# Performance work log

Measured on AMD Instinct MI355X. Metric: run time of the kernel, lower is better.

The kernel has to match this reference:

```python
import jax, jax.numpy as jnp
import numpy as np

B, S, H, F, E, K = 2, 2048, 1024, 4096, 8, 2


def setup_inputs() -> dict:
    key = jax.random.key(0)
    ks = jax.random.split(key, 5)
    scale = 0.02
    return {
        "hidden_states": jax.random.normal(ks[0], (B, S, H), jnp.float32),
        "gate_w": jax.random.normal(ks[1], (H, E), jnp.float32) * scale,  # nn.Linear(H,E,bias=False)
        "w1": jax.random.normal(ks[2], (E, H, F), jnp.float32) * scale,   # per-expert fc1
        "b1": jnp.zeros((E, F), jnp.float32),
        "w2": jax.random.normal(ks[3], (E, F, H), jnp.float32) * scale,   # per-expert fc2
        "b2": jnp.zeros((E, H), jnp.float32),
    }


def reference(hidden_states, gate_w, w1, b1, w2, b2):
    b, s, h = hidden_states.shape
    x = hidden_states.reshape(b * s, h)  # [T, H]
    T = x.shape[0]
    n_experts = gate_w.shape[1]

    # --- Top-K gating ---
    router_logits = x @ gate_w                      # [T, E]
    router_probs = jax.nn.softmax(router_logits, axis=-1)
    topk_probs, topk_idx = jax.lax.top_k(router_probs, K)  # [T, K]
    topk_probs = topk_probs / topk_probs.sum(axis=-1, keepdims=True)
    aux_loss = n_experts * jnp.sum(router_probs.mean(axis=0) ** 2)

    # --- Combine weights: scatter normalized top-k probs into dense [T, E] ---
    combine_w = jnp.zeros((T, n_experts), x.dtype).at[
        jnp.arange(T)[:, None], topk_idx
    ].add(topk_probs)

    # --- Expert MLPs (dense per-expert batched GEMM; zero combine weight drops unrouted) ---
    hidden = jax.nn.relu(jnp.einsum('th,ehf->etf', x, w1) + b1[:, None, :])  # [E, T, F]
    expert_out = jnp.einsum('etf,efh->eth', hidden, w2) + b2[:, None, :]     # [E, T, H]

    out = jnp.einsum('te,eth->th', combine_w, expert_out)  # weighted combine
    return out.reshape(b, s, h), aux_loss
```

## Files before the change

### kernel.cpp

```cpp
#include <hip/hip_runtime.h>
#include <hip/hip_bf16.h>
#include <cstdint>

#define AS1 __attribute__((address_space(1)))
#define AS3 __attribute__((address_space(3)))

typedef __attribute__((ext_vector_type(8))) short short8x;
typedef __attribute__((ext_vector_type(4))) float f32x4;

static constexpr int T    = 4096;
static constexpr int HD   = 1024;
static constexpr int FD   = 4096;
static constexpr int NE   = 8;
static constexpr int P    = T * 2;
static constexpr int PPAD = P + 128;
static constexpr int MAXT = P / 128 + NE;
static constexpr int RTB  = 16;
static constexpr int RNB  = T / RTB;

struct TileDesc { int e; int start; int rows; int pad; };

__device__ __forceinline__ uint16_t f2bf(float f) {
  uint32_t u = __builtin_bit_cast(uint32_t, f);
  u += 0x7FFFu + ((u >> 16) & 1u);
  return (uint16_t)(u >> 16);
}
__device__ __forceinline__ float bf2f(uint16_t b) {
  uint32_t u = ((uint32_t)b) << 16;
  return __builtin_bit_cast(float, u);
}
__device__ __forceinline__ void gload_lds16(const void* g, void* l) {
  __builtin_amdgcn_global_load_lds((const AS1 uint32_t*)g, (AS3 uint32_t*)l, 16, 0, 0);
}

__global__ __launch_bounds__(256) void cvt_x_kernel(const float* __restrict__ x,
                                                    uint16_t* __restrict__ xb) {
  size_t i = ((size_t)blockIdx.x * 256 + threadIdx.x) * 4;
  float4 v = *(const float4*)&x[i];
  ushort4 o;
  o.x = f2bf(v.x); o.y = f2bf(v.y); o.z = f2bf(v.z); o.w = f2bf(v.w);
  *(ushort4*)&xb[i] = o;
}

__global__ __launch_bounds__(256) void transpose_cvt_kernel(
    const float* __restrict__ in, uint16_t* __restrict__ out, int R, int C) {
  __shared__ float tile[64][65];
  int z = blockIdx.z;
  const float* inp = in + (size_t)z * R * C;
  uint16_t* outp = out + (size_t)z * R * C;
  int r0 = blockIdx.y * 64, c0 = blockIdx.x * 64;
  int tid = threadIdx.x;
  int lr = tid >> 4;
  int lc4 = (tid & 15) * 4;
#pragma unroll
  for (int p = 0; p < 4; ++p) {
    float4 v = *(const float4*)&inp[(size_t)(r0 + lr + p * 16) * C + c0 + lc4];
    tile[lr + p * 16][lc4 + 0] = v.x;
    tile[lr + p * 16][lc4 + 1] = v.y;
    tile[lr + p * 16][lc4 + 2] = v.z;
    tile[lr + p * 16][lc4 + 3] = v.w;
  }
  __syncthreads();
#pragma unroll
  for (int p = 0; p < 4; ++p) {
    int c = lr + p * 16;
    ushort4 o;
    o.x = f2bf(tile[lc4 + 0][c]);
    o.y = f2bf(tile[lc4 + 1][c]);
    o.z = f2bf(tile[lc4 + 2][c]);
    o.w = f2bf(tile[lc4 + 3][c]);
    *(ushort4*)&outp[(size_t)(c0 + c) * R + r0 + lc4] = o;
  }
}

__global__ __launch_bounds__(256) void router_kernel(
    const float* __restrict__ x, const float* __restrict__ gate_w,
    int* __restrict__ topk_idx, float* __restrict__ topk_w,
    float* __restrict__ part_sums, int* __restrict__ part_counts) {
  __shared__ float g[NE * HD];
  __shared__ float ls[NE];
  __shared__ int   lc[NE];
  int tid = threadIdx.x;
  for (int i = tid; i < NE * HD; i += 256)
    g[(i & 7) * HD + (i >> 3)] = gate_w[i];
  if (tid < NE) { ls[tid] = 0.f; lc[tid] = 0; }
  __syncthreads();
  int wave = tid >> 6, lane = tid & 63;
  float psum[NE];
#pragma unroll
  for (int e = 0; e < NE; ++e) psum[e] = 0.f;

  for (int tt = 0; tt < RTB / 4; ++tt) {
    int t = blockIdx.x * RTB + wave * (RTB / 4) + tt;
    const float* xr = x + (size_t)t * HD;
    float acc[NE];
#pragma unroll
    for (int e = 0; e < NE; ++e) acc[e] = 0.f;
    for (int i = 0; i < HD / 64; ++i) {
      float xv = xr[lane + i * 64];
#pragma unroll
      for (int e = 0; e < NE; ++e) acc[e] += xv * g[e * HD + lane + i * 64];
    }
#pragma unroll
    for (int off = 32; off > 0; off >>= 1)
#pragma unroll
      for (int e = 0; e < NE; ++e) acc[e] += __shfl_down(acc[e], off);
    if (lane == 0) {
      float m = acc[0];
#pragma unroll
      for (int e = 1; e < NE; ++e) m = fmaxf(m, acc[e]);
      float p[NE], s = 0.f;
#pragma unroll
      for (int e = 0; e < NE; ++e) { p[e] = expf(acc[e] - m); s += p[e]; }
      float inv = 1.f / s;
#pragma unroll
      for (int e = 0; e < NE; ++e) { p[e] *= inv; psum[e] += p[e]; }
      int i0 = 0;
#pragma unroll
      for (int e = 1; e < NE; ++e) if (p[e] > p[i0]) i0 = e;
      int i1 = (i0 == 0) ? 1 : 0;
#pragma unroll
      for (int e = 0; e < NE; ++e) if (e != i0 && e != i1 && p[e] > p[i1]) i1 = e;
      float wsum = p[i0] + p[i1];
      topk_idx[t * 2] = i0; topk_idx[t * 2 + 1] = i1;
      topk_w[t * 2] = p[i0] / wsum; topk_w[t * 2 + 1] = p[i1] / wsum;
      atomicAdd(&lc[i0], 1); atomicAdd(&lc[i1], 1);
    }
  }
  if (lane == 0)
#pragma unroll
    for (int e = 0; e < NE; ++e) atomicAdd(&ls[e], psum[e]);
  __syncthreads();
  if (tid < NE) {
    part_sums[blockIdx.x * NE + tid]   = ls[tid];
    part_counts[blockIdx.x * NE + tid] = lc[tid];
  }
}

__global__ __launch_bounds__(64) void finalize_kernel(
    const int* __restrict__ part_counts, const float* __restrict__ part_sums,
    int* __restrict__ offsets, TileDesc* __restrict__ desc,
    int* __restrict__ ntiles, float* __restrict__ aux_out) {
  __shared__ int   csh[NE];
  __shared__ float ssh[NE];
  int tid = threadIdx.x;
  if (tid < NE) {
    int c = 0; float s = 0.f;
    for (int b = 0; b < RNB; ++b) {
      c += part_counts[b * NE + tid];
      s += part_sums[b * NE + tid];
    }
    csh[tid] = c; ssh[tid] = s;
  }
  __syncthreads();
  if (tid == 0) {
    int off = 0, nt = 0;
    for (int e = 0; e < NE; ++e) {
      offsets[e] = off;
      int c = csh[e];
      for (int i = 0; i < c; i += 128) {
        int rows = c - i; if (rows > 128) rows = 128;
        desc[nt].e = e; desc[nt].start = off + i; desc[nt].rows = rows; desc[nt].pad = 0;
        nt++;
      }
      off += c;
    }
    *ntiles = nt;
    float aux = 0.f;
    for (int e = 0; e < NE; ++e) {
      float mean = ssh[e] / (float)T;
      aux += mean * mean;
    }
    *aux_out = (float)NE * aux;
  }
}

__global__ __launch_bounds__(256) void scatter_kernel(
    const int* __restrict__ topk_idx, const int* __restrict__ offsets,
    int* __restrict__ fill, int* __restrict__ pair_tok, int* __restrict__ tok_pos) {
  int t = blockIdx.x * 256 + threadIdx.x;
  int lane = threadIdx.x & 63;
  unsigned long long below = (lane == 63) ? ~0ull >> 1
                                          : ((1ull << (lane + 1)) - 1) >> 1;
#pragma unroll
  for (int k = 0; k < 2; ++k) {
    int e = topk_idx[t * 2 + k];
    int pos = 0;
    for (int ex = 0; ex < NE; ++ex) {
      unsigned long long m = __ballot(e == ex);
      if (e == ex) {
        int leader = __ffsll((long long)m) - 1;
        int cnt = __popcll(m);
        int base = 0;
        if (lane == leader) base = atomicAdd(&fill[ex], cnt);
        base = __shfl(base, leader);
        pos = base + __popcll(m & below);
      }
    }
    int pp = offsets[e] + pos;
    pair_tok[pp] = t;
    tok_pos[t * 2 + k] = pp;
  }
}

template <int KD, int ND, int NBG, int EPI>
__global__ __launch_bounds__(256) void moe_gemm(
    const uint16_t* __restrict__ Abase, const int* __restrict__ pair_tok,
    const uint16_t* __restrict__ Bw, const float* __restrict__ bias,
    uint16_t* __restrict__ Cout, const TileDesc* __restrict__ desc,
    const int* __restrict__ ntiles) {
  constexpr int NB = ND / 128;
  constexpr int SM = MAXT / 8;

  int orig = blockIdx.x;
  int xcd = orig & 7, local = orig >> 3;
  int nbq = local / (SM * NBG);
  int rem = local % (SM * NBG);
  int mt  = xcd * SM + rem / NBG;
  int nb  = nbq * NBG + rem % NBG;
  if (mt >= *ntiles) return;
  TileDesc d = desc[mt];

  __shared__ uint16_t As[128 * 32];
  __shared__ uint16_t Bs[128 * 32];
  __shared__ int rowA[128];

  int tid = threadIdx.x, lane = tid & 63, wave = tid >> 6;
  int wm = wave >> 1, wn = wave & 1;

  int idx0 = (wave * 2 + 0) * 64 + lane;
  int idx1 = (wave * 2 + 1) * 64 + lane;
  int ar0 = idx0 >> 2, kc0 = idx0 & 3;
  int ar1 = idx1 >> 2, kc1 = idx1 & 3;

  int ra0, ra1;
  if constexpr (EPI == 0) {
    if (tid < 128) rowA[tid] = (tid < d.rows) ? pair_tok[d.start + tid] : 0;
    __syncthreads();
    ra0 = rowA[ar0]; ra1 = rowA[ar1];
  } else {
    ra0 = d.start + ar0; ra1 = d.start + ar1;
  }

  const uint16_t* Bbase = Bw + ((size_t)d.e * ND + (size_t)nb * 128) * KD;

  f32x4 acc[4][4];
#pragma unroll
  for (int i = 0; i < 4; ++i)
#pragma unroll
    for (int j = 0; j < 4; ++j) acc[i][j] = (f32x4){0.f, 0.f, 0.f, 0.f};

  for (int kt = 0; kt < KD / 32; ++kt) {
    if (kt) __syncthreads();
    int kb = kt * 32;
    gload_lds16(Abase + (size_t)ra0 * KD + kb + kc0 * 8, &As[(wave * 2 + 0) * 512]);
    gload_lds16(Abase + (size_t)ra1 * KD + kb + kc1 * 8, &As[(wave * 2 + 1) * 512]);
    gload_lds16(Bbase + (size_t)ar0 * KD + kb + kc0 * 8, &Bs[(wave * 2 + 0) * 512]);
    gload_lds16(Bbase + (size_t)ar1 * KD + kb + kc1 * 8, &Bs[(wave * 2 + 1) * 512]);
    __syncthreads();

    short8x af[4], bfr[4];
#pragma unroll
    for (int i = 0; i < 4; ++i)
      af[i] = *(const short8x*)&As[(wm * 64 + i * 16 + (lane & 15)) * 32 + (lane >> 4) * 8];
#pragma unroll
    for (int j = 0; j < 4; ++j)
      bfr[j] = *(const short8x*)&Bs[(wn * 64 + j * 16 + (lane & 15)) * 32 + (lane >> 4) * 8];
#pragma unroll
    for (int i = 0; i < 4; ++i)
#pragma unroll
      for (int j = 0; j < 4; ++j)
        acc[i][j] = __builtin_amdgcn_mfma_f32_16x16x32_bf16(af[i], bfr[j], acc[i][j], 0, 0, 0);
  }

  int rq = (lane >> 4) * 4;
  int cl = lane & 15;
#pragma unroll
  for (int i = 0; i < 4; ++i) {
    int rb = wm * 64 + i * 16 + rq;
#pragma unroll
    for (int j = 0; j < 4; ++j) {
      int col = nb * 128 + wn * 64 + j * 16 + cl;
      float bv = bias[d.e * ND + col];
#pragma unroll
      for (int q = 0; q < 4; ++q) {
        int r = rb + q;
        if (r < d.rows) {
          float v = acc[i][j][q] + bv;
          if (EPI == 0) v = fmaxf(v, 0.f);
          Cout[(size_t)(d.start + r) * ND + col] = f2bf(v);
        }
      }
    }
  }
}

__global__ __launch_bounds__(256) void combine_kernel(
    const uint16_t* __restrict__ po, const int* __restrict__ tok_pos,
    const float* __restrict__ topk_w, float* __restrict__ out) {
  int t = blockIdx.x;
  int c = threadIdx.x * 4;
  int p0 = tok_pos[t * 2], p1 = tok_pos[t * 2 + 1];
  float w0 = topk_w[t * 2], w1 = topk_w[t * 2 + 1];
  ushort4 a = *(const ushort4*)&po[(size_t)p0 * HD + c];
  ushort4 b = *(const ushort4*)&po[(size_t)p1 * HD + c];
  float4 o;
  o.x = w0 * bf2f(a.x) + w1 * bf2f(b.x);
  o.y = w0 * bf2f(a.y) + w1 * bf2f(b.y);
  o.z = w0 * bf2f(a.z) + w1 * bf2f(b.z);
  o.w = w0 * bf2f(a.w) + w1 * bf2f(b.w);
  *(float4*)&out[(size_t)t * HD + c] = o;
}

extern "C" void kernel_launch(void* const* d_in, const int* in_sizes, int n_in,
                              void* d_out, int out_size, void* d_ws, size_t ws_size,
                              hipStream_t stream) {
  const float* x      = (const float*)d_in[0];
  const float* gate_w = (const float*)d_in[1];
  const float* w1     = (const float*)d_in[2];
  const float* b1     = (const float*)d_in[3];
  const float* w2     = (const float*)d_in[4];
  const float* b2     = (const float*)d_in[5];
  float* out = (float*)d_out;
  (void)in_sizes; (void)n_in; (void)out_size; (void)ws_size;

  char* w = (char*)d_ws;
  size_t off = 0;
  auto alloc = [&](size_t bytes) -> void* {
    void* p = w + off;
    off = (off + bytes + 255) & ~(size_t)255;
    return p;
  };
  int*      meta     = (int*)alloc(256);
  int*      fill     = meta;
  int*      offsets  = (int*)alloc(256);
  int*      ntiles   = offsets + 8;
  TileDesc* desc     = (TileDesc*)alloc(sizeof(TileDesc) * 128);
  int*      topk_idx = (int*)alloc(sizeof(int) * P);
  float*    topk_w   = (float*)alloc(sizeof(float) * P);
  int*      tok_pos  = (int*)alloc(sizeof(int) * P);
  int*      pair_tok = (int*)alloc(sizeof(int) * PPAD);
  float*    psums    = (float*)alloc(sizeof(float) * RNB * NE);
  int*      pcounts  = (int*)alloc(sizeof(int) * RNB * NE);
  uint16_t* xb       = (uint16_t*)alloc((size_t)T * HD * 2);
  uint16_t* w1t      = (uint16_t*)alloc((size_t)NE * FD * HD * 2);
  uint16_t* w2t      = (uint16_t*)alloc((size_t)NE * HD * FD * 2);
  uint16_t* hidden   = (uint16_t*)alloc((size_t)PPAD * FD * 2);
  uint16_t* pout     = (uint16_t*)alloc((size_t)PPAD * HD * 2);

  hipMemsetAsync(meta, 0, 256, stream);
  cvt_x_kernel<<<(T * HD) / 1024, 256, 0, stream>>>(x, xb);
  transpose_cvt_kernel<<<dim3(FD / 64, HD / 64, NE), 256, 0, stream>>>(w1, w1t, HD, FD);
  transpose_cvt_kernel<<<dim3(HD / 64, FD / 64, NE), 256, 0, stream>>>(w2, w2t, FD, HD);
  router_kernel<<<RNB, 256, 0, stream>>>(x, gate_w, topk_idx, topk_w, psums, pcounts);
  finalize_kernel<<<1, 64, 0, stream>>>(pcounts, psums, offsets, desc, ntiles,
                                        out + (size_t)T * HD);
  scatter_kernel<<<T / 256, 256, 0, stream>>>(topk_idx, offsets, fill, pair_tok, tok_pos);
  moe_gemm<HD, FD, 4, 0><<<(FD / 128) * MAXT, 256, 0, stream>>>(
      xb, pair_tok, w1t, b1, hidden, desc, ntiles);
  moe_gemm<FD, HD, 8, 1><<<(HD / 128) * MAXT, 256, 0, stream>>>(
      hidden, pair_tok, w2t, b2, pout, desc, ntiles);
  combine_kernel<<<T, 256, 0, stream>>>(pout, tok_pos, topk_w, out);
}
```

Before: 370.5 us.

## Split-K the down-projection GEMM and swizzle LDS tiles to avoid bank conflicts

The second expert GEMM is split into two K halves, doubling its grid. Each half writes fp32 partials into a buffer that reuses the transposed w1 storage, and the combine kernel sums the two halves. Both GEMMs also get an XOR swizzle on LDS column chunks, applied at global-load time and matched on the fragment reads, to reduce LDS bank conflicts. In exchange, the partial outputs double the write and read traffic through fp32 buffers.

New measurement: 381.0 us. 2.8% more time.

```diff
diff --git a/kernel.cpp b/kernel.cpp
--- a/kernel.cpp
+++ b/kernel.cpp
@@ -203,23 +203,25 @@
   }
 }
 
-template <int KD, int ND, int NBG, int EPI>
+template <int KSTRIDE, int KLEN, int ND, int NBG, int KH, int EPI>
 __global__ __launch_bounds__(256) void moe_gemm(
     const uint16_t* __restrict__ Abase, const int* __restrict__ pair_tok,
     const uint16_t* __restrict__ Bw, const float* __restrict__ bias,
-    uint16_t* __restrict__ Cout, const TileDesc* __restrict__ desc,
+    void* __restrict__ CoutV, const TileDesc* __restrict__ desc,
     const int* __restrict__ ntiles) {
-  constexpr int NB = ND / 128;
   constexpr int SM = MAXT / 8;
 
   int orig = blockIdx.x;
   int xcd = orig & 7, local = orig >> 3;
-  int nbq = local / (SM * NBG);
-  int rem = local % (SM * NBG);
+  int kh  = local % KH;
+  int l2  = local / KH;
+  int nbq = l2 / (SM * NBG);
+  int rem = l2 % (SM * NBG);
   int mt  = xcd * SM + rem / NBG;
   int nb  = nbq * NBG + rem % NBG;
   if (mt >= *ntiles) return;
   TileDesc d = desc[mt];
+  const int kOff = kh * KLEN;
 
   __shared__ uint16_t As[128 * 32];
   __shared__ uint16_t Bs[128 * 32];
@@ -228,10 +230,11 @@
   int tid = threadIdx.x, lane = tid & 63, wave = tid >> 6;
   int wm = wave >> 1, wn = wave & 1;
 
-  int idx0 = (wave * 2 + 0) * 64 + lane;
-  int idx1 = (wave * 2 + 1) * 64 + lane;
+  int idx0 = wave * 128 + lane;
   int ar0 = idx0 >> 2, kc0 = idx0 & 3;
-  int ar1 = idx1 >> 2, kc1 = idx1 & 3;
+  int ar1 = ar0 + 16;
+  int fsw = (ar0 & 3) ^ ((ar0 >> 2) & 3);
+  int scol = (kc0 ^ fsw) * 8;
 
   int ra0, ra1;
   if constexpr (EPI == 0) {
@@ -242,7 +245,11 @@
     ra0 = d.start + ar0; ra1 = d.start + ar1;
   }
 
-  const uint16_t* Bbase = Bw + ((size_t)d.e * ND + (size_t)nb * 128) * KD;
+  const uint16_t* Bbase = Bw + ((size_t)d.e * ND + (size_t)nb * 128) * KSTRIDE + kOff;
+  const uint16_t* Ar0 = Abase + (size_t)ra0 * KSTRIDE + kOff + scol;
+  const uint16_t* Ar1 = Abase + (size_t)ra1 * KSTRIDE + kOff + scol;
+  const uint16_t* Br0 = Bbase + (size_t)ar0 * KSTRIDE + scol;
+  const uint16_t* Br1 = Bbase + (size_t)ar1 * KSTRIDE + scol;
 
   f32x4 acc[4][4];
 #pragma unroll
@@ -250,22 +257,25 @@
 #pragma unroll
     for (int j = 0; j < 4; ++j) acc[i][j] = (f32x4){0.f, 0.f, 0.f, 0.f};
 
-  for (int kt = 0; kt < KD / 32; ++kt) {
+  int swr = (((lane >> 4) ^ (lane & 3) ^ ((lane >> 2) & 3)) << 3);
+  int l15 = lane & 15;
+
+  for (int kt = 0; kt < KLEN / 32; ++kt) {
     if (kt) __syncthreads();
     int kb = kt * 32;
-    gload_lds16(Abase + (size_t)ra0 * KD + kb + kc0 * 8, &As[(wave * 2 + 0) * 512]);
-    gload_lds16(Abase + (size_t)ra1 * KD + kb + kc1 * 8, &As[(wave * 2 + 1) * 512]);
-    gload_lds16(Bbase + (size_t)ar0 * KD + kb + kc0 * 8, &Bs[(wave * 2 + 0) * 512]);
-    gload_lds16(Bbase + (size_t)ar1 * KD + kb + kc1 * 8, &Bs[(wave * 2 + 1) * 512]);
+    gload_lds16(Ar0 + kb, &As[(wave * 2 + 0) * 512]);
+    gload_lds16(Ar1 + kb, &As[(wave * 2 + 1) * 512]);
+    gload_lds16(Br0 + kb, &Bs[(wave * 2 + 0) * 512]);
+    gload_lds16(Br1 + kb, &Bs[(wave * 2 + 1) * 512]);
     __syncthreads();
 
     short8x af[4], bfr[4];
 #pragma unroll
     for (int i = 0; i < 4; ++i)
-      af[i] = *(const short8x*)&As[(wm * 64 + i * 16 + (lane & 15)) * 32 + (lane >> 4) * 8];
+      af[i] = *(const short8x*)&As[(wm * 64 + i * 16 + l15) * 32 + swr];
 #pragma unroll
     for (int j = 0; j < 4; ++j)
-      bfr[j] = *(const short8x*)&Bs[(wn * 64 + j * 16 + (lane & 15)) * 32 + (lane >> 4) * 8];
+      bfr[j] = *(const short8x*)&Bs[(wn * 64 + j * 16 + l15) * 32 + swr];
 #pragma unroll
     for (int i = 0; i < 4; ++i)
 #pragma unroll
@@ -281,14 +291,18 @@
 #pragma unroll
     for (int j = 0; j < 4; ++j) {
       int col = nb * 128 + wn * 64 + j * 16 + cl;
-      float bv = bias[d.e * ND + col];
+      float bv = (EPI == 1 && kh != 0) ? 0.f : bias[d.e * ND + col];
 #pragma unroll
       for (int q = 0; q < 4; ++q) {
         int r = rb + q;
         if (r < d.rows) {
           float v = acc[i][j][q] + bv;
-          if (EPI == 0) v = fmaxf(v, 0.f);
-          Cout[(size_t)(d.start + r) * ND + col] = f2bf(v);
+          if constexpr (EPI == 0) {
+            v = fmaxf(v, 0.f);
+            ((uint16_t*)CoutV)[(size_t)(d.start + r) * ND + col] = f2bf(v);
+          } else {
+            ((float*)CoutV)[(size_t)kh * P * ND + (size_t)(d.start + r) * ND + col] = v;
+          }
         }
       }
     }
@@ -296,19 +310,22 @@
 }
 
 __global__ __launch_bounds__(256) void combine_kernel(
-    const uint16_t* __restrict__ po, const int* __restrict__ tok_pos,
+    const float* __restrict__ po, const int* __restrict__ tok_pos,
     const float* __restrict__ topk_w, float* __restrict__ out) {
   int t = blockIdx.x;
   int c = threadIdx.x * 4;
   int p0 = tok_pos[t * 2], p1 = tok_pos[t * 2 + 1];
   float w0 = topk_w[t * 2], w1 = topk_w[t * 2 + 1];
-  ushort4 a = *(const ushort4*)&po[(size_t)p0 * HD + c];
-  ushort4 b = *(const ushort4*)&po[(size_t)p1 * HD + c];
+  const float* h1 = po + (size_t)P * HD;
+  float4 a0 = *(const float4*)&po[(size_t)p0 * HD + c];
+  float4 a1 = *(const float4*)&h1[(size_t)p0 * HD + c];
+  float4 b0 = *(const float4*)&po[(size_t)p1 * HD + c];
+  float4 b1 = *(const float4*)&h1[(size_t)p1 * HD + c];
   float4 o;
-  o.x = w0 * bf2f(a.x) + w1 * bf2f(b.x);
-  o.y = w0 * bf2f(a.y) + w1 * bf2f(b.y);
-  o.z = w0 * bf2f(a.z) + w1 * bf2f(b.z);
-  o.w = w0 * bf2f(a.w) + w1 * bf2f(b.w);
+  o.x = w0 * (a0.x + a1.x) + w1 * (b0.x + b1.x);
+  o.y = w0 * (a0.y + a1.y) + w1 * (b0.y + b1.y);
+  o.z = w0 * (a0.z + a1.z) + w1 * (b0.z + b1.z);
+  o.w = w0 * (a0.w + a1.w) + w1 * (b0.w + b1.w);
   *(float4*)&out[(size_t)t * HD + c] = o;
 }
 
@@ -346,7 +363,7 @@
   uint16_t* w1t      = (uint16_t*)alloc((size_t)NE * FD * HD * 2);
   uint16_t* w2t      = (uint16_t*)alloc((size_t)NE * HD * FD * 2);
   uint16_t* hidden   = (uint16_t*)alloc((size_t)PPAD * FD * 2);
-  uint16_t* pout     = (uint16_t*)alloc((size_t)PPAD * HD * 2);
+  float*    pout     = (float*)w1t;
 
   hipMemsetAsync(meta, 0, 256, stream);
   cvt_x_kernel<<<(T * HD) / 1024, 256, 0, stream>>>(x, xb);
@@ -356,9 +373,9 @@
   finalize_kernel<<<1, 64, 0, stream>>>(pcounts, psums, offsets, desc, ntiles,
                                         out + (size_t)T * HD);
   scatter_kernel<<<T / 256, 256, 0, stream>>>(topk_idx, offsets, fill, pair_tok, tok_pos);
-  moe_gemm<HD, FD, 4, 0><<<(FD / 128) * MAXT, 256, 0, stream>>>(
+  moe_gemm<HD, HD, FD, 4, 1, 0><<<(FD / 128) * MAXT, 256, 0, stream>>>(
       xb, pair_tok, w1t, b1, hidden, desc, ntiles);
-  moe_gemm<FD, HD, 8, 1><<<(HD / 128) * MAXT, 256, 0, stream>>>(
-      hidden, pair_tok, w2t, b2, pout, desc, ntiles);
+  moe_gemm<FD, FD / 2, HD, 8, 2, 1><<<(HD / 128) * MAXT * 2, 256, 0, stream>>>(
+      hidden, nullptr, w2t, b2, pout, desc, ntiles);
   combine_kernel<<<T, 256, 0, stream>>>(pout, tok_pos, topk_w, out);
 }
```

## Fuse weight transpose and bf16 conversion into MoE GEMM B-tile loads

Applied to the files above, without the earlier changes.

Drops the two transpose_cvt pre-pass kernels that converted w1/w2 to transposed bf16 copies. Each GEMM block now reads fp32 weights directly, converts them to bf16 in registers and writes them into the LDS B tile with a transposed pair-packed layout. This removes a full read/write pass over all expert weights (~128MB of fp32 read plus bf16 writes). The cost is that each weight tile is re-read as fp32 by every M-tile that uses it, doubling B traffic per GEMM. B loads also become synchronous register loads plus scattered LDS stores that may bank-conflict, instead of async global-to-LDS copies.

After: 528.0 us. 42.5% more time.

```diff
diff --git a/kernel.cpp b/kernel.cpp
--- a/kernel.cpp
+++ b/kernel.cpp
@@ -40,37 +40,6 @@
   ushort4 o;
   o.x = f2bf(v.x); o.y = f2bf(v.y); o.z = f2bf(v.z); o.w = f2bf(v.w);
   *(ushort4*)&xb[i] = o;
-}
-
-__global__ __launch_bounds__(256) void transpose_cvt_kernel(
-    const float* __restrict__ in, uint16_t* __restrict__ out, int R, int C) {
-  __shared__ float tile[64][65];
-  int z = blockIdx.z;
-  const float* inp = in + (size_t)z * R * C;
-  uint16_t* outp = out + (size_t)z * R * C;
-  int r0 = blockIdx.y * 64, c0 = blockIdx.x * 64;
-  int tid = threadIdx.x;
-  int lr = tid >> 4;
-  int lc4 = (tid & 15) * 4;
-#pragma unroll
-  for (int p = 0; p < 4; ++p) {
-    float4 v = *(const float4*)&inp[(size_t)(r0 + lr + p * 16) * C + c0 + lc4];
-    tile[lr + p * 16][lc4 + 0] = v.x;
-    tile[lr + p * 16][lc4 + 1] = v.y;
-    tile[lr + p * 16][lc4 + 2] = v.z;
-    tile[lr + p * 16][lc4 + 3] = v.w;
-  }
-  __syncthreads();
-#pragma unroll
-  for (int p = 0; p < 4; ++p) {
-    int c = lr + p * 16;
-    ushort4 o;
-    o.x = f2bf(tile[lc4 + 0][c]);
-    o.y = f2bf(tile[lc4 + 1][c]);
-    o.z = f2bf(tile[lc4 + 2][c]);
-    o.w = f2bf(tile[lc4 + 3][c]);
-    *(ushort4*)&outp[(size_t)(c0 + c) * R + r0 + lc4] = o;
-  }
 }
 
 __global__ __launch_bounds__(256) void router_kernel(
@@ -206,10 +175,9 @@
 template <int KD, int ND, int NBG, int EPI>
 __global__ __launch_bounds__(256) void moe_gemm(
     const uint16_t* __restrict__ Abase, const int* __restrict__ pair_tok,
-    const uint16_t* __restrict__ Bw, const float* __restrict__ bias,
+    const float* __restrict__ W, const float* __restrict__ bias,
     uint16_t* __restrict__ Cout, const TileDesc* __restrict__ desc,
     const int* __restrict__ ntiles) {
-  constexpr int NB = ND / 128;
   constexpr int SM = MAXT / 8;
 
   int orig = blockIdx.x;
@@ -242,7 +210,9 @@
     ra0 = d.start + ar0; ra1 = d.start + ar1;
   }
 
-  const uint16_t* Bbase = Bw + ((size_t)d.e * ND + (size_t)nb * 128) * KD;
+  int bkr = (tid & 15) * 2;
+  int bnc = (tid >> 4) * 8;
+  const float* Wb = W + (size_t)d.e * KD * ND + (size_t)nb * 128 + bnc;
 
   f32x4 acc[4][4];
 #pragma unroll
@@ -253,10 +223,22 @@
   for (int kt = 0; kt < KD / 32; ++kt) {
     if (kt) __syncthreads();
     int kb = kt * 32;
+    const float* w0r = Wb + (size_t)(kb + bkr) * ND;
+    const float* w1r = w0r + ND;
+    float4 a0 = *(const float4*)(w0r);
+    float4 a1 = *(const float4*)(w0r + 4);
+    float4 b0 = *(const float4*)(w1r);
+    float4 b1 = *(const float4*)(w1r + 4);
     gload_lds16(Abase + (size_t)ra0 * KD + kb + kc0 * 8, &As[(wave * 2 + 0) * 512]);
     gload_lds16(Abase + (size_t)ra1 * KD + kb + kc1 * 8, &As[(wave * 2 + 1) * 512]);
-    gload_lds16(Bbase + (size_t)ar0 * KD + kb + kc0 * 8, &Bs[(wave * 2 + 0) * 512]);
-    gload_lds16(Bbase + (size_t)ar1 * KD + kb + kc1 * 8, &Bs[(wave * 2 + 1) * 512]);
+    uint32_t* bsw = (uint32_t*)Bs;
+    float r0[8] = {a0.x, a0.y, a0.z, a0.w, a1.x, a1.y, a1.z, a1.w};
+    float r1[8] = {b0.x, b0.y, b0.z, b0.w, b1.x, b1.y, b1.z, b1.w};
+#pragma unroll
+    for (int j = 0; j < 8; ++j) {
+      uint32_t pk = (uint32_t)f2bf(r0[j]) | ((uint32_t)f2bf(r1[j]) << 16);
+      bsw[((bnc + j) * 32 + bkr) >> 1] = pk;
+    }
     __syncthreads();
 
     short8x af[4], bfr[4];
@@ -343,22 +325,18 @@
   float*    psums    = (float*)alloc(sizeof(float) * RNB * NE);
   int*      pcounts  = (int*)alloc(sizeof(int) * RNB * NE);
   uint16_t* xb       = (uint16_t*)alloc((size_t)T * HD * 2);
-  uint16_t* w1t      = (uint16_t*)alloc((size_t)NE * FD * HD * 2);
-  uint16_t* w2t      = (uint16_t*)alloc((size_t)NE * HD * FD * 2);
   uint16_t* hidden   = (uint16_t*)alloc((size_t)PPAD * FD * 2);
   uint16_t* pout     = (uint16_t*)alloc((size_t)PPAD * HD * 2);
 
   hipMemsetAsync(meta, 0, 256, stream);
   cvt_x_kernel<<<(T * HD) / 1024, 256, 0, stream>>>(x, xb);
-  transpose_cvt_kernel<<<dim3(FD / 64, HD / 64, NE), 256, 0, stream>>>(w1, w1t, HD, FD);
-  transpose_cvt_kernel<<<dim3(HD / 64, FD / 64, NE), 256, 0, stream>>>(w2, w2t, FD, HD);
   router_kernel<<<RNB, 256, 0, stream>>>(x, gate_w, topk_idx, topk_w, psums, pcounts);
   finalize_kernel<<<1, 64, 0, stream>>>(pcounts, psums, offsets, desc, ntiles,
                                         out + (size_t)T * HD);
   scatter_kernel<<<T / 256, 256, 0, stream>>>(topk_idx, offsets, fill, pair_tok, tok_pos);
   moe_gemm<HD, FD, 4, 0><<<(FD / 128) * MAXT, 256, 0, stream>>>(
-      xb, pair_tok, w1t, b1, hidden, desc, ntiles);
+      xb, pair_tok, w1, b1, hidden, desc, ntiles);
   moe_gemm<FD, HD, 8, 1><<<(HD / 128) * MAXT, 256, 0, stream>>>(
-      hidden, pair_tok, w2t, b2, pout, desc, ntiles);
+      hidden, pair_tok, w2, b2, pout, desc, ntiles);
   combine_kernel<<<T, 256, 0, stream>>>(pout, tok_pos, topk_w, out);
 }
```

## Merge prep kernels and overlap w2 transpose with fc1 GEMM via block roles

Applied to the files above, without the earlier changes.

Folds the x conversion, the w1 transpose/convert and the router into one prep launch that dispatches on block index. It also appends the w2 transpose blocks to the fc1 GEMM launch, so that conversion can overlap with GEMM work instead of running as a separate serial kernel. This cuts launch count and lets memory-bound transpose work fill idle CUs. The cost is a larger shared-memory footprint per kernel, from the router's 33KB buffer and the unified 17KB buffer, which may lower occupancy. Block scheduling order may also make the transpose blocks trail the GEMM blocks rather than overlap with them.

New measurement: 377.6 us. About the same (+1.9%).

```diff
diff --git a/kernel.cpp b/kernel.cpp
--- a/kernel.cpp
+++ b/kernel.cpp
@@ -18,6 +18,11 @@
 static constexpr int RTB  = 16;
 static constexpr int RNB  = T / RTB;
 
+static constexpr int TW1G = (FD / 64) * (HD / 64) * NE;
+static constexpr int CVTG = (T * HD) / 1024;
+static constexpr int FC1G = (FD / 128) * MAXT;
+static constexpr int TW2G = (HD / 64) * (FD / 64) * NE;
+
 struct TileDesc { int e; int start; int rows; int pad; };
 
 __device__ __forceinline__ uint16_t f2bf(float f) {
@@ -33,53 +38,58 @@
   __builtin_amdgcn_global_load_lds((const AS1 uint32_t*)g, (AS3 uint32_t*)l, 16, 0, 0);
 }
 
-__global__ __launch_bounds__(256) void cvt_x_kernel(const float* __restrict__ x,
-                                                    uint16_t* __restrict__ xb) {
-  size_t i = ((size_t)blockIdx.x * 256 + threadIdx.x) * 4;
+__device__ __forceinline__ void transpose_role(
+    const float* __restrict__ in, uint16_t* __restrict__ out,
+    int R, int C, int bi, float* tile ) {
+  int nbc = C / 64;
+  int nbr = R / 64;
+  int cx = bi % nbc;
+  int ry = (bi / nbc) % nbr;
+  int z  = bi / (nbc * nbr);
+  const float* inp = in + (size_t)z * R * C;
+  uint16_t* outp = out + (size_t)z * R * C;
+  int r0 = ry * 64, c0 = cx * 64;
+  int tid = threadIdx.x;
+  int lr = tid >> 4;
+  int lc4 = (tid & 15) * 4;
+#pragma unroll
+  for (int p = 0; p < 4; ++p) {
+    float4 v = *(const float4*)&inp[(size_t)(r0 + lr + p * 16) * C + c0 + lc4];
+    tile[(lr + p * 16) * 65 + lc4 + 0] = v.x;
+    tile[(lr + p * 16) * 65 + lc4 + 1] = v.y;
+    tile[(lr + p * 16) * 65 + lc4 + 2] = v.z;
+    tile[(lr + p * 16) * 65 + lc4 + 3] = v.w;
+  }
+  __syncthreads();
+#pragma unroll
+  for (int p = 0; p < 4; ++p) {
+    int c = lr + p * 16;
+    ushort4 o;
+    o.x = f2bf(tile[(lc4 + 0) * 65 + c]);
+    o.y = f2bf(tile[(lc4 + 1) * 65 + c]);
+    o.z = f2bf(tile[(lc4 + 2) * 65 + c]);
+    o.w = f2bf(tile[(lc4 + 3) * 65 + c]);
+    *(ushort4*)&outp[(size_t)(c0 + c) * R + r0 + lc4] = o;
+  }
+}
+
+__device__ __forceinline__ void cvt_role(const float* __restrict__ x,
+                                         uint16_t* __restrict__ xb, int bi) {
+  size_t i = ((size_t)bi * 256 + threadIdx.x) * 4;
   float4 v = *(const float4*)&x[i];
   ushort4 o;
   o.x = f2bf(v.x); o.y = f2bf(v.y); o.z = f2bf(v.z); o.w = f2bf(v.w);
   *(ushort4*)&xb[i] = o;
 }
 
-__global__ __launch_bounds__(256) void transpose_cvt_kernel(
-    const float* __restrict__ in, uint16_t* __restrict__ out, int R, int C) {
-  __shared__ float tile[64][65];
-  int z = blockIdx.z;
-  const float* inp = in + (size_t)z * R * C;
-  uint16_t* outp = out + (size_t)z * R * C;
-  int r0 = blockIdx.y * 64, c0 = blockIdx.x * 64;
-  int tid = threadIdx.x;
-  int lr = tid >> 4;
-  int lc4 = (tid & 15) * 4;
-#pragma unroll
-  for (int p = 0; p < 4; ++p) {
-    float4 v = *(const float4*)&inp[(size_t)(r0 + lr + p * 16) * C + c0 + lc4];
-    tile[lr + p * 16][lc4 + 0] = v.x;
-    tile[lr + p * 16][lc4 + 1] = v.y;
-    tile[lr + p * 16][lc4 + 2] = v.z;
-    tile[lr + p * 16][lc4 + 3] = v.w;
-  }
-  __syncthreads();
-#pragma unroll
-  for (int p = 0; p < 4; ++p) {
-    int c = lr + p * 16;
-    ushort4 o;
-    o.x = f2bf(tile[lc4 + 0][c]);
-    o.y = f2bf(tile[lc4 + 1][c]);
-    o.z = f2bf(tile[lc4 + 2][c]);
-    o.w = f2bf(tile[lc4 + 3][c]);
-    *(ushort4*)&outp[(size_t)(c0 + c) * R + r0 + lc4] = o;
-  }
-}
-
-__global__ __launch_bounds__(256) void router_kernel(
+__device__ __forceinline__ void router_role(
     const float* __restrict__ x, const float* __restrict__ gate_w,
     int* __restrict__ topk_idx, float* __restrict__ topk_w,
-    float* __restrict__ part_sums, int* __restrict__ part_counts) {
-  __shared__ float g[NE * HD];
-  __shared__ float ls[NE];
-  __shared__ int   lc[NE];
+    float* __restrict__ part_sums, int* __restrict__ part_counts,
+    int rb, char* smem) {
+  float* g  = (float*)smem;
+  float* ls = (float*)(smem + 32768);
+  int*   lc = (int*)(smem + 32768 + 32);
   int tid = threadIdx.x;
   for (int i = tid; i < NE * HD; i += 256)
     g[(i & 7) * HD + (i >> 3)] = gate_w[i];
@@ -91,7 +101,7 @@
   for (int e = 0; e < NE; ++e) psum[e] = 0.f;
 
   for (int tt = 0; tt < RTB / 4; ++tt) {
-    int t = blockIdx.x * RTB + wave * (RTB / 4) + tt;
+    int t = rb * RTB + wave * (RTB / 4) + tt;
     const float* xr = x + (size_t)t * HD;
     float acc[NE];
 #pragma unroll
@@ -132,8 +142,26 @@
     for (int e = 0; e < NE; ++e) atomicAdd(&ls[e], psum[e]);
   __syncthreads();
   if (tid < NE) {
-    part_sums[blockIdx.x * NE + tid]   = ls[tid];
-    part_counts[blockIdx.x * NE + tid] = lc[tid];
+    part_sums[rb * NE + tid]   = ls[tid];
+    part_counts[rb * NE + tid] = lc[tid];
+  }
+}
+
+__global__ __launch_bounds__(256) void prep_kernel(
+    const float* __restrict__ x, const float* __restrict__ gate_w,
+    const float* __restrict__ w1,
+    uint16_t* __restrict__ xb, uint16_t* __restrict__ w1t,
+    int* __restrict__ topk_idx, float* __restrict__ topk_w,
+    float* __restrict__ part_sums, int* __restrict__ part_counts) {
+  __shared__ __align__(16) char smem[33024];
+  int b = blockIdx.x;
+  if (b < TW1G) {
+    transpose_role(w1, w1t, HD, FD, b, (float*)smem);
+  } else if (b < TW1G + CVTG) {
+    cvt_role(x, xb, b - TW1G);
+  } else {
+    router_role(x, gate_w, topk_idx, topk_w, part_sums, part_counts,
+                b - TW1G - CVTG, smem);
   }
 }
 
@@ -204,15 +232,14 @@
 }
 
 template <int KD, int ND, int NBG, int EPI>
-__global__ __launch_bounds__(256) void moe_gemm(
+__device__ __forceinline__ void gemm_role(
+    char* smem, int orig,
     const uint16_t* __restrict__ Abase, const int* __restrict__ pair_tok,
     const uint16_t* __restrict__ Bw, const float* __restrict__ bias,
     uint16_t* __restrict__ Cout, const TileDesc* __restrict__ desc,
     const int* __restrict__ ntiles) {
-  constexpr int NB = ND / 128;
   constexpr int SM = MAXT / 8;
 
-  int orig = blockIdx.x;
   int xcd = orig & 7, local = orig >> 3;
   int nbq = local / (SM * NBG);
   int rem = local % (SM * NBG);
@@ -221,9 +248,9 @@
   if (mt >= *ntiles) return;
   TileDesc d = desc[mt];
 
-  __shared__ uint16_t As[128 * 32];
-  __shared__ uint16_t Bs[128 * 32];
-  __shared__ int rowA[128];
+  uint16_t* As = (uint16_t*)smem;
+  uint16_t* Bs = (uint16_t*)(smem + 8192);
+  int* rowA    = (int*)(smem + 16384);
 
   int tid = threadIdx.x, lane = tid & 63, wave = tid >> 6;
   int wm = wave >> 1, wn = wave & 1;
@@ -293,6 +320,29 @@
       }
     }
   }
+}
+
+__global__ __launch_bounds__(256) void fc1_fused_kernel(
+    const uint16_t* __restrict__ xb, const int* __restrict__ pair_tok,
+    const uint16_t* __restrict__ w1t, const float* __restrict__ b1,
+    uint16_t* __restrict__ hidden, const TileDesc* __restrict__ desc,
+    const int* __restrict__ ntiles,
+    const float* __restrict__ w2, uint16_t* __restrict__ w2t) {
+  __shared__ __align__(16) char smem[17408];
+  int b = blockIdx.x;
+  if (b < FC1G) {
+    gemm_role<HD, FD, 4, 0>(smem, b, xb, pair_tok, w1t, b1, hidden, desc, ntiles);
+  } else {
+    transpose_role(w2, w2t, FD, HD, b - FC1G, (float*)smem);
+  }
+}
+
+__global__ __launch_bounds__(256) void fc2_kernel(
+    const uint16_t* __restrict__ hidden, const uint16_t* __restrict__ w2t,
+    const float* __restrict__ b2, uint16_t* __restrict__ pout,
+    const TileDesc* __restrict__ desc, const int* __restrict__ ntiles) {
+  __shared__ __align__(16) char smem[17408];
+  gemm_role<FD, HD, 8, 1>(smem, blockIdx.x, hidden, nullptr, w2t, b2, pout, desc, ntiles);
 }
 
 __global__ __launch_bounds__(256) void combine_kernel(
@@ -349,16 +399,14 @@
   uint16_t* pout     = (uint16_t*)alloc((size_t)PPAD * HD * 2);
 
   hipMemsetAsync(meta, 0, 256, stream);
-  cvt_x_kernel<<<(T * HD) / 1024, 256, 0, stream>>>(x, xb);
-  transpose_cvt_kernel<<<dim3(FD / 64, HD / 64, NE), 256, 0, stream>>>(w1, w1t, HD, FD);
-  transpose_cvt_kernel<<<dim3(HD / 64, FD / 64, NE), 256, 0, stream>>>(w2, w2t, FD, HD);
-  router_kernel<<<RNB, 256, 0, stream>>>(x, gate_w, topk_idx, topk_w, psums, pcounts);
+  prep_kernel<<<TW1G + CVTG + RNB, 256, 0, stream>>>(
+      x, gate_w, w1, xb, w1t, topk_idx, topk_w, psums, pcounts);
   finalize_kernel<<<1, 64, 0, stream>>>(pcounts, psums, offsets, desc, ntiles,
                                         out + (size_t)T * HD);
   scatter_kernel<<<T / 256, 256, 0, stream>>>(topk_idx, offsets, fill, pair_tok, tok_pos);
-  moe_gemm<HD, FD, 4, 0><<<(FD / 128) * MAXT, 256, 0, stream>>>(
-      xb, pair_tok, w1t, b1, hidden, desc, ntiles);
-  moe_gemm<FD, HD, 8, 1><<<(HD / 128) * MAXT, 256, 0, stream>>>(
-      hidden, pair_tok, w2t, b2, pout, desc, ntiles);
+  fc1_fused_kernel<<<FC1G + TW2G, 256, 0, stream>>>(
+      xb, pair_tok, w1t, b1, hidden, desc, ntiles, w2, w2t);
+  fc2_kernel<<<(HD / 128) * MAXT, 256, 0, stream>>>(
+      hidden, w2t, b2, pout, desc, ntiles);
   combine_kernel<<<T, 256, 0, stream>>>(pout, tok_pos, topk_w, out);
 }
```
